# Performance work log

Measured on AMD Instinct MI355X. Metric: run time of the kernel, lower is better.

The kernel has to match this reference:

```python
import jax, jax.numpy as jnp
import numpy as np

N_HEAD = 16
N_EMBD = 768
HEAD_DIM = N_EMBD // N_HEAD  # 48


def setup_inputs() -> dict:
    key = jax.random.key(0)
    k1, k2, k3 = jax.random.split(key, 3)
    B, T, C = 4, 2048, N_EMBD
    x = jax.random.normal(k1, (B, T, C), dtype=jnp.float32)
    # nn.Linear(n_embd, 3*n_embd, bias=False): y = x @ W_attn, stored as [C, 3C]
    W_attn = jax.random.normal(k2, (C, 3 * C), dtype=jnp.float32) * (C ** -0.5)
    W_proj = jax.random.normal(k3, (C, C), dtype=jnp.float32) * (C ** -0.5)
    b_proj = jnp.zeros((C,), dtype=jnp.float32)
    return {"x": x, "W_attn": W_attn, "W_proj": W_proj, "b_proj": b_proj}


def reference(x, W_attn, W_proj, b_proj):
    B, T, C = x.shape
    qkv = x @ W_attn  # [B, T, 3C]
    q, k, v = jnp.split(qkv, 3, axis=-1)
    # [B, T, H, D]
    q = q.reshape(B, T, N_HEAD, HEAD_DIM)
    k = k.reshape(B, T, N_HEAD, HEAD_DIM)
    v = v.reshape(B, T, N_HEAD, HEAD_DIM)
    scale = HEAD_DIM ** -0.5
    # scores: [B, H, Tq, Tk]
    wei = jnp.einsum("bqhd,bkhd->bhqk", q, k) * scale
    causal = jnp.tril(jnp.ones((T, T), dtype=bool))
    wei = jnp.where(causal[None, None, :, :], wei, -jnp.inf)
    wei = jax.nn.softmax(wei, axis=-1)
    # dropout omitted (eval mode / deterministic reference)
    out = jnp.einsum("bhqk,bkhd->bqhd", wei, v).reshape(B, T, C)
    return out @ W_proj + b_proj
```

## Files before the change

### kernel.cpp

```cpp
#include <hip/hip_runtime.h>
#include <cstdint>
#include <cstddef>

#define B_ 4
#define T_ 2048
#define C_ 768
#define H_ 16
#define D_ 48
#define M_ (B_*T_)
#define N3_ (3*C_)

typedef unsigned short u16;
typedef __attribute__((ext_vector_type(8))) short bf16x8;
typedef __attribute__((ext_vector_type(4))) float f32x4;
typedef __attribute__((ext_vector_type(4))) unsigned int u32x4;
typedef __attribute__((ext_vector_type(4))) unsigned short u16x4;

typedef const __attribute__((address_space(1))) unsigned int* gptr_t;
typedef __attribute__((address_space(3))) unsigned int* lptr_t;

__device__ __forceinline__ u16 f2b(float f){
  union { float f; unsigned u; } x; x.f = f;
  unsigned u = x.u;
  return (u16)((u + 0x7FFFu + ((u >> 16) & 1u)) >> 16);
}

__device__ __forceinline__ unsigned cvtpk(float lo, float hi){
  unsigned r;
  asm("v_cvt_pk_bf16_f32 %0, %1, %2" : "=v"(r) : "v"(lo), "v"(hi));
  return r;
}

__device__ __forceinline__ bf16x8 ld_frag(const u16* lds, int row, int kbyte){
  const char* p = (const char*)lds + (row << 7) + (kbyte ^ ((row & 7) << 4));
  return *(const bf16x8*)p;
}

__device__ __forceinline__ bf16x8 ld_k(const u16* kb, int rbase, int off){
  return *(const bf16x8*)((const char*)kb + rbase + off);
}

__global__ void k_cvt(const float* __restrict__ in, u16* __restrict__ out, int n4){
  int i = blockIdx.x * blockDim.x + threadIdx.x;
  if (i >= n4) return;
  f32x4 v = *(const f32x4*)(in + 4*(size_t)i);
  u16x4 o;
  o.x = f2b(v.x); o.y = f2b(v.y); o.z = f2b(v.z); o.w = f2b(v.w);
  *(u16x4*)(out + 4*(size_t)i) = o;
}

__global__ void k_tpose(const float* __restrict__ in, u16* __restrict__ out, int R, int Cn,
                        int scaleRows, float scl){
  __shared__ float tile[32][33];
  int tx = threadIdx.x & 31, ty = threadIdx.x >> 5;
  int c  = blockIdx.x * 32 + tx;
  int rb = blockIdx.y * 32;
  #pragma unroll
  for (int r0 = 0; r0 < 32; r0 += 8)
    tile[ty + r0][tx] = in[(size_t)(rb + ty + r0) * Cn + c];
  __syncthreads();
  int oc = rb + tx;
  int cb = blockIdx.x * 32;
  #pragma unroll
  for (int r0 = 0; r0 < 32; r0 += 8){
    float v = tile[tx][ty + r0];
    if (cb + ty + r0 < scaleRows) v *= scl;
    out[(size_t)(cb + ty + r0) * R + oc] = f2b(v);
  }
}

template<bool OUT_BF16, bool ADD_BIAS>
__launch_bounds__(256)
__global__ void k_gemm(const u16* __restrict__ A, const u16* __restrict__ Bt,
                       void* __restrict__ Cout, const float* __restrict__ bias,
                       int Ndim, int Kdim){
  __shared__ u16 lA[128*64];
  __shared__ u16 lB[128*64];
  const int tid = threadIdx.x, lane = tid & 63, w = tid >> 6;
  const int m0 = blockIdx.x * 128, n0 = blockIdx.y * 128;
  const int wr = (w >> 1) * 64, wc = (w & 1) * 64;
  const f32x4 fzero = {0.f, 0.f, 0.f, 0.f};
  f32x4 acc[4][4];
  #pragma unroll
  for (int i = 0; i < 4; ++i)
    #pragma unroll
    for (int j = 0; j < 4; ++j) acc[i][j] = fzero;

  for (int k0 = 0; k0 < Kdim; k0 += 64){
    __syncthreads();
    #pragma unroll
    for (int it = 0; it < 4; ++it){
      int c = tid + it * 256;
      int row  = c >> 3;
      int cb   = (c & 7) << 4;
      int pcol = cb ^ ((row & 7) << 4);
      const char* ga = (const char*)(A  + (size_t)(m0 + row) * Kdim + k0) + pcol;
      const char* gb = (const char*)(Bt + (size_t)(n0 + row) * Kdim + k0) + pcol;
      __builtin_amdgcn_global_load_lds((gptr_t)ga, (lptr_t)((char*)lA + (c << 4)), 16, 0, 0);
      __builtin_amdgcn_global_load_lds((gptr_t)gb, (lptr_t)((char*)lB + (c << 4)), 16, 0, 0);
    }
    __syncthreads();
    #pragma unroll
    for (int kk = 0; kk < 2; ++kk){
      int kbyte = (kk << 6) + ((lane >> 4) << 4);
      bf16x8 af[4], bfv[4];
      #pragma unroll
      for (int i = 0; i < 4; ++i){
        af[i]  = ld_frag(lA, wr + i*16 + (lane & 15), kbyte);
        bfv[i] = ld_frag(lB, wc + i*16 + (lane & 15), kbyte);
      }
      #pragma unroll
      for (int i = 0; i < 4; ++i)
        #pragma unroll
        for (int j = 0; j < 4; ++j)
          acc[i][j] = __builtin_amdgcn_mfma_f32_16x16x32_bf16(af[i], bfv[j], acc[i][j], 0, 0, 0);
    }
  }
  #pragma unroll
  for (int i = 0; i < 4; ++i){
    int rbase = m0 + wr + i*16 + ((lane >> 4) << 2);
    #pragma unroll
    for (int j = 0; j < 4; ++j){
      int col = n0 + wc + j*16 + (lane & 15);
      float bv = ADD_BIAS ? bias[col] : 0.f;
      #pragma unroll
      for (int r = 0; r < 4; ++r){
        float v = acc[i][j][r] + bv;
        if (OUT_BF16) ((u16*)Cout)[(size_t)(rbase + r) * Ndim + col] = f2b(v);
        else          ((float*)Cout)[(size_t)(rbase + r) * Ndim + col] = v;
      }
    }
  }
}

__global__ void k_vt(const u16* __restrict__ qkv, u16* __restrict__ vt){
  __shared__ u16 tl[64][50];
  int t0 = blockIdx.x * 64;
  int bh = blockIdx.y; int b = bh >> 4, h = bh & 15;
  int tid = threadIdx.x;
  for (int i = tid; i < 64*48; i += 256){
    int tt = i / 48, d = i % 48;
    tl[tt][d] = qkv[(size_t)(b*T_ + t0 + tt) * N3_ + 2*C_ + h*D_ + d];
  }
  __syncthreads();
  for (int i = tid; i < 48*64; i += 256){
    int d = i >> 6, tt = i & 63;
    vt[(size_t)(bh*D_ + d) * T_ + t0 + tt] = tl[tt][d];
  }
}

__launch_bounds__(256)
__global__ void k_attn(const u16* __restrict__ qkv, const u16* __restrict__ vt,
                       u16* __restrict__ ao){
  __shared__ u16 lKV[2][2][6144];

  const int wg = ((blockIdx.x & 7) << 7) + (blockIdx.x >> 3);
  const int q  = wg & 127;
  const int pairI = q >> 3;
  const int bh = ((wg >> 7) << 3) + (q & 7);
  const int qbA = pairI, qbB = 31 - pairI;
  const int b = bh >> 4, h = bh & 15;
  const int tid = threadIdx.x, lane = tid & 63, w = tid >> 6;
  const int ls = lane & 15, hi = lane >> 4;
  const int krb = ls * 96 + hi * 16;
  const f32x4 fzero = {0.f, 0.f, 0.f, 0.f};
  const bf16x8 bzero = {0, 0, 0, 0, 0, 0, 0, 0};

  bf16x8 aqA[2], aqB[2];
  {
    const u16* qpA = qkv + (size_t)(b*T_ + qbA*64 + w*16 + ls) * N3_ + h*D_ + hi*8;
    aqA[0] = *(const bf16x8*)qpA;
    aqA[1] = (hi < 2) ? *(const bf16x8*)(qpA + 32) : bzero;
    const u16* qpB = qkv + (size_t)(b*T_ + qbB*64 + w*16 + ls) * N3_ + h*D_ + hi*8;
    aqB[0] = *(const bf16x8*)qpB;
    aqB[1] = (hi < 2) ? *(const bf16x8*)(qpB + 32) : bzero;
  }

  const char* kg0; const char* kg1; const char* vg;
  {
    int c0 = tid,       r0 = c0 / 6, i0 = (c0 % 6) << 4;
    int c1 = tid + 256, r1 = c1 / 6, i1 = (c1 % 6) << 4;
    kg0 = (const char*)(qkv + (size_t)(b*T_ + r0) * N3_ + C_ + h*D_) + i0;
    kg1 = (const char*)(qkv + (size_t)(b*T_ + r1) * N3_ + C_ + h*D_) + i1;
    int d0  = tid >> 5;
    int pb4 = (tid << 2) & 127;
    int lb  = pb4 ^ (d0 << 4);
    int k   = lb >> 1;
    int sk  = (k & 0x23) | ((k & 4) << 2) | ((k & 0x18) >> 1);
    vg = (const char*)(vt + (size_t)(bh*D_ + d0) * T_) + (sk << 1);
  }
  const size_t kstep = (size_t)64 * N3_ * 2;

  auto STAGE1 = [&](int s, int buf, int sl){
    const size_t ko = (size_t)s * kstep;
    const int vo = s * 128;
    char* base = (char*)&lKV[buf][sl][0];
    __builtin_amdgcn_global_load_lds((gptr_t)(kg0 + ko), (lptr_t)(base + (tid << 4)), 16, 0, 0);
    if (tid < 128)
      __builtin_amdgcn_global_load_lds((gptr_t)(kg1 + ko), (lptr_t)(base + ((tid + 256) << 4)), 16, 0, 0);
    char* vd = base + 6144;
    #pragma unroll
    for (int it = 0; it < 6; ++it)
      __builtin_amdgcn_global_load_lds((gptr_t)(vg + vo + it * (8 * T_ * 2)),
          (lptr_t)(vd + ((tid + it*256) << 2)), 4, 0, 0);
  };

  float lsumA = 0.f, lsumB = 0.f;
  f32x4 oaccA[3], oaccB[3];
  #pragma unroll
  for (int nf = 0; nf < 3; ++nf){ oaccA[nf] = fzero; oaccB[nf] = fzero; }

  int cur = 0;

  auto softmax = [&](f32x4 (&s)[4], float &lsum,
                     bf16x8 &pb0, bf16x8 &pb1, bool diag, int krow0, int qt){
    if (diag){
      int qg = qt + w*16 + ls;
      #pragma unroll
      for (int nf = 0; nf < 4; ++nf)
        #pragma unroll
        for (int r = 0; r < 4; ++r){
          int kg2 = krow0 + nf*16 + hi*4 + r;
          s[nf][r] = (kg2 <= qg) ? s[nf][r] : -1e30f;
        }
    }
    float p[4][4];
    #pragma unroll
    for (int nf = 0; nf < 4; ++nf)
      #pragma unroll
      for (int r = 0; r < 4; ++r){
        float e = __builtin_amdgcn_exp2f(fminf(s[nf][r], 60.f));
        p[nf][r] = e;
        lsum += e;
      }
    union { u32x4 u; bf16x8 b; } w0, w1;
    w0.u.x = cvtpk(p[0][0], p[0][1]); w0.u.y = cvtpk(p[0][2], p[0][3]);
    w0.u.z = cvtpk(p[1][0], p[1][1]); w0.u.w = cvtpk(p[1][2], p[1][3]);
    w1.u.x = cvtpk(p[2][0], p[2][1]); w1.u.y = cvtpk(p[2][2], p[2][3]);
    w1.u.z = cvtpk(p[3][0], p[3][1]); w1.u.w = cvtpk(p[3][2], p[3][3]);
    pb0 = w0.b; pb1 = w1.b;
  };

  auto process = [&](int ks, int sl){
    const bool actA = (ks <= qbA);
    const u16* Kb = &lKV[cur][sl][0];
    const u16* Vb = Kb + 3072;

    f32x4 stA[4], stB[4];
    #pragma unroll
    for (int nf = 0; nf < 4; ++nf){ stA[nf] = fzero; stB[nf] = fzero; }
    #pragma unroll
    for (int kk = 0; kk < 2; ++kk){
      #pragma unroll
      for (int nf = 0; nf < 4; ++nf){
        bf16x8 bk = ld_k(Kb, krb, nf*1536 + (kk << 6));
        stB[nf] = __builtin_amdgcn_mfma_f32_16x16x32_bf16(bk, aqB[kk], stB[nf], 0, 0, 0);
        if (actA)
          stA[nf] = __builtin_amdgcn_mfma_f32_16x16x32_bf16(bk, aqA[kk], stA[nf], 0, 0, 0);
      }
    }

    bf16x8 pbA0, pbA1, pbB0, pbB1;
    if (actA) softmax(stA, lsumA, pbA0, pbA1, ks == qbA, ks*64, qbA*64);
    softmax(stB, lsumB, pbB0, pbB1, ks == qbB, ks*64, qbB*64);

    #pragma unroll
    for (int kk = 0; kk < 2; ++kk){
      int kbyte = (kk << 6) + (hi << 4);
      #pragma unroll
      for (int nf = 0; nf < 3; ++nf){
        bf16x8 bv = ld_frag(Vb, nf*16 + ls, kbyte);
        oaccB[nf] = __builtin_amdgcn_mfma_f32_16x16x32_bf16(
            bv, kk ? pbB1 : pbB0, oaccB[nf], 0, 0, 0);
        if (actA)
          oaccA[nf] = __builtin_amdgcn_mfma_f32_16x16x32_bf16(
              bv, kk ? pbA1 : pbA0, oaccA[nf], 0, 0, 0);
      }
    }
  };

  const int kb2max = qbB >> 1;
  STAGE1(0, 0, 0);
  if (qbB >= 1) STAGE1(1, 0, 1);
  __syncthreads();

  for (int kb2 = 0; kb2 <= kb2max; ++kb2){
    if (kb2 < kb2max){
      STAGE1(2*kb2 + 2, cur ^ 1, 0);
      if (2*kb2 + 3 <= qbB) STAGE1(2*kb2 + 3, cur ^ 1, 1);
    }

    process(2*kb2, 0);
    if (2*kb2 + 1 <= qbB) process(2*kb2 + 1, 1);

    if (kb2 < kb2max){
      __syncthreads();
      cur ^= 1;
    }
  }

  float lA = lsumA; lA += __shfl_xor(lA, 16); lA += __shfl_xor(lA, 32);
  float lB = lsumB; lB += __shfl_xor(lB, 16); lB += __shfl_xor(lB, 32);
  float invA = 1.f / lA, invB = 1.f / lB;
  int tA = qbA*64 + w*16 + ls, tB = qbB*64 + w*16 + ls;
  #pragma unroll
  for (int nf = 0; nf < 3; ++nf){
    u16x4 oA, oB;
    #pragma unroll
    for (int r = 0; r < 4; ++r){
      oA[r] = f2b(oaccA[nf][r] * invA);
      oB[r] = f2b(oaccB[nf][r] * invB);
    }
    int col = h*D_ + nf*16 + hi*4;
    *(u16x4*)(ao + (size_t)(b*T_ + tA) * C_ + col) = oA;
    *(u16x4*)(ao + (size_t)(b*T_ + tB) * C_ + col) = oB;
  }
}

extern "C" void kernel_launch(void* const* d_in, const int* in_sizes, int n_in,
                              void* d_out, int out_size, void* d_ws, size_t ws_size,
                              hipStream_t stream){
  if (n_in < 4) return;
  const float* x      = (const float*)d_in[0];
  const float* W_attn = (const float*)d_in[1];
  const float* W_proj = (const float*)d_in[2];
  const float* b_proj = (const float*)d_in[3];

  char* ws = (char*)d_ws;
  size_t off = 0;
  auto alloc = [&](size_t bytes)->void*{
    void* p = ws + off; off += (bytes + 255) & ~(size_t)255; return p;
  };
  u16* xb   = (u16*)alloc((size_t)M_ * C_  * 2);
  u16* wabT = (u16*)alloc((size_t)N3_ * C_ * 2);
  u16* wpbT = (u16*)alloc((size_t)C_ * C_  * 2);
  u16* qkv  = (u16*)alloc((size_t)M_ * N3_ * 2);
  u16* vt   = (u16*)alloc((size_t)B_ * H_ * D_ * T_ * 2);
  u16* ao   = (u16*)alloc((size_t)M_ * C_  * 2);
  if (off > ws_size) return;

  const float scale2 = 0.20823527f;

  k_cvt<<<dim3((M_*C_/4 + 255)/256), dim3(256), 0, stream>>>(x, xb, M_*C_/4);
  k_tpose<<<dim3(N3_/32, C_/32), dim3(256), 0, stream>>>(W_attn, wabT, C_, N3_, C_, scale2);
  k_tpose<<<dim3(C_/32,  C_/32), dim3(256), 0, stream>>>(W_proj, wpbT, C_, C_, 0, 1.f);
  k_gemm<true,false><<<dim3(M_/128, N3_/128), dim3(256), 0, stream>>>(
      xb, wabT, (void*)qkv, (const float*)nullptr, N3_, C_);
  k_vt<<<dim3(T_/64, B_*H_), dim3(256), 0, stream>>>(qkv, vt);
  k_attn<<<dim3(1024), dim3(256), 0, stream>>>(qkv, vt, ao);
  k_gemm<false,true><<<dim3(M_/128, C_/128), dim3(256), 0, stream>>>(
      ao, wpbT, d_out, b_proj, C_, C_);
}
```

Measured before the change: 140.2 us.

## Merge preprocessing kernels into one launch and shrink GEMM tiles to 64x128

The x bf16 conversion and both weight transposes now run in a single launch, split by block index ranges, which removes two kernel launches and their gaps. Both GEMMs now use 64x128 tiles, with each wave computing a 64x32 slice, in place of 128x128 tiles. This doubles the block count for better CU occupancy, especially for the projection GEMM's small grid, at the cost of less data reuse per block and more redundant B-tile loads.

```diff
diff --git a/kernel.cpp b/kernel.cpp
--- a/kernel.cpp
+++ b/kernel.cpp
@@ -40,27 +40,19 @@
   return *(const bf16x8*)((const char*)kb + rbase + off);
 }
 
-__global__ void k_cvt(const float* __restrict__ in, u16* __restrict__ out, int n4){
-  int i = blockIdx.x * blockDim.x + threadIdx.x;
-  if (i >= n4) return;
-  f32x4 v = *(const f32x4*)(in + 4*(size_t)i);
-  u16x4 o;
-  o.x = f2b(v.x); o.y = f2b(v.y); o.z = f2b(v.z); o.w = f2b(v.w);
-  *(u16x4*)(out + 4*(size_t)i) = o;
-}
-
-__global__ void k_tpose(const float* __restrict__ in, u16* __restrict__ out, int R, int Cn,
-                        int scaleRows, float scl){
+__device__ __forceinline__ void tpose_body(const float* __restrict__ in,
+                                           u16* __restrict__ out, int R, int Cn,
+                                           int bx, int by, int scaleRows, float scl){
   __shared__ float tile[32][33];
   int tx = threadIdx.x & 31, ty = threadIdx.x >> 5;
-  int c  = blockIdx.x * 32 + tx;
-  int rb = blockIdx.y * 32;
+  int c  = bx * 32 + tx;
+  int rb = by * 32;
   #pragma unroll
   for (int r0 = 0; r0 < 32; r0 += 8)
     tile[ty + r0][tx] = in[(size_t)(rb + ty + r0) * Cn + c];
   __syncthreads();
   int oc = rb + tx;
-  int cb = blockIdx.x * 32;
+  int cb = bx * 32;
   #pragma unroll
   for (int r0 = 0; r0 < 32; r0 += 8){
     float v = tile[tx][ty + r0];
@@ -69,59 +61,82 @@
   }
 }
 
+__global__ void k_prep(const float* __restrict__ x, u16* __restrict__ xb,
+                       const float* __restrict__ Wa, u16* __restrict__ wabT,
+                       const float* __restrict__ Wp, u16* __restrict__ wpbT,
+                       float scl){
+  int blk = blockIdx.x;
+  if (blk < 6144){
+    int i = blk * 256 + threadIdx.x;
+    f32x4 v = *(const f32x4*)(x + 4*(size_t)i);
+    u16x4 o;
+    o.x = f2b(v.x); o.y = f2b(v.y); o.z = f2b(v.z); o.w = f2b(v.w);
+    *(u16x4*)(xb + 4*(size_t)i) = o;
+  } else if (blk < 7872){
+    int id = blk - 6144;
+    tpose_body(Wa, wabT, C_, N3_, id % 72, id / 72, C_, scl);
+  } else {
+    int id = blk - 7872;
+    tpose_body(Wp, wpbT, C_, C_, id % 24, id / 24, 0, 1.f);
+  }
+}
+
 template<bool OUT_BF16, bool ADD_BIAS>
 __launch_bounds__(256)
-__global__ void k_gemm(const u16* __restrict__ A, const u16* __restrict__ Bt,
-                       void* __restrict__ Cout, const float* __restrict__ bias,
-                       int Ndim, int Kdim){
-  __shared__ u16 lA[128*64];
+__global__ void k_gemm2(const u16* __restrict__ A, const u16* __restrict__ Bt,
+                        void* __restrict__ Cout, const float* __restrict__ bias,
+                        int Ndim, int Kdim){
+  __shared__ u16 lA[64*64];
   __shared__ u16 lB[128*64];
   const int tid = threadIdx.x, lane = tid & 63, w = tid >> 6;
-  const int m0 = blockIdx.x * 128, n0 = blockIdx.y * 128;
-  const int wr = (w >> 1) * 64, wc = (w & 1) * 64;
+  const int m0 = blockIdx.x * 64, n0 = blockIdx.y * 128;
+  const int wc = w * 32;
+  const int ls = lane & 15, hi = lane >> 4;
   const f32x4 fzero = {0.f, 0.f, 0.f, 0.f};
-  f32x4 acc[4][4];
-  #pragma unroll
-  for (int i = 0; i < 4; ++i)
-    #pragma unroll
-    for (int j = 0; j < 4; ++j) acc[i][j] = fzero;
+  f32x4 acc[4][2];
+  #pragma unroll
+  for (int i = 0; i < 4; ++i){ acc[i][0] = fzero; acc[i][1] = fzero; }
 
   for (int k0 = 0; k0 < Kdim; k0 += 64){
     __syncthreads();
     #pragma unroll
+    for (int it = 0; it < 2; ++it){
+      int c = tid + it * 256;
+      int row = c >> 3, cb = (c & 7) << 4;
+      int pcol = cb ^ ((row & 7) << 4);
+      const char* ga = (const char*)(A + (size_t)(m0 + row) * Kdim + k0) + pcol;
+      __builtin_amdgcn_global_load_lds((gptr_t)ga, (lptr_t)((char*)lA + (c << 4)), 16, 0, 0);
+    }
+    #pragma unroll
     for (int it = 0; it < 4; ++it){
       int c = tid + it * 256;
-      int row  = c >> 3;
-      int cb   = (c & 7) << 4;
+      int row = c >> 3, cb = (c & 7) << 4;
       int pcol = cb ^ ((row & 7) << 4);
-      const char* ga = (const char*)(A  + (size_t)(m0 + row) * Kdim + k0) + pcol;
       const char* gb = (const char*)(Bt + (size_t)(n0 + row) * Kdim + k0) + pcol;
-      __builtin_amdgcn_global_load_lds((gptr_t)ga, (lptr_t)((char*)lA + (c << 4)), 16, 0, 0);
       __builtin_amdgcn_global_load_lds((gptr_t)gb, (lptr_t)((char*)lB + (c << 4)), 16, 0, 0);
     }
     __syncthreads();
     #pragma unroll
     for (int kk = 0; kk < 2; ++kk){
-      int kbyte = (kk << 6) + ((lane >> 4) << 4);
-      bf16x8 af[4], bfv[4];
-      #pragma unroll
-      for (int i = 0; i < 4; ++i){
-        af[i]  = ld_frag(lA, wr + i*16 + (lane & 15), kbyte);
-        bfv[i] = ld_frag(lB, wc + i*16 + (lane & 15), kbyte);
-      }
+      int kbyte = (kk << 6) + (hi << 4);
+      bf16x8 af[4], bfv[2];
+      #pragma unroll
+      for (int i = 0; i < 4; ++i) af[i] = ld_frag(lA, i*16 + ls, kbyte);
+      #pragma unroll
+      for (int j = 0; j < 2; ++j) bfv[j] = ld_frag(lB, wc + j*16 + ls, kbyte);
       #pragma unroll
       for (int i = 0; i < 4; ++i)
         #pragma unroll
-        for (int j = 0; j < 4; ++j)
+        for (int j = 0; j < 2; ++j)
           acc[i][j] = __builtin_amdgcn_mfma_f32_16x16x32_bf16(af[i], bfv[j], acc[i][j], 0, 0, 0);
     }
   }
   #pragma unroll
   for (int i = 0; i < 4; ++i){
-    int rbase = m0 + wr + i*16 + ((lane >> 4) << 2);
-    #pragma unroll
-    for (int j = 0; j < 4; ++j){
-      int col = n0 + wc + j*16 + (lane & 15);
+    int rbase = m0 + i*16 + (hi << 2);
+    #pragma unroll
+    for (int j = 0; j < 2; ++j){
+      int col = n0 + wc + j*16 + ls;
       float bv = ADD_BIAS ? bias[col] : 0.f;
       #pragma unroll
       for (int r = 0; r < 4; ++r){
@@ -341,13 +356,11 @@
 
   const float scale2 = 0.20823527f;
 
-  k_cvt<<<dim3((M_*C_/4 + 255)/256), dim3(256), 0, stream>>>(x, xb, M_*C_/4);
-  k_tpose<<<dim3(N3_/32, C_/32), dim3(256), 0, stream>>>(W_attn, wabT, C_, N3_, C_, scale2);
-  k_tpose<<<dim3(C_/32,  C_/32), dim3(256), 0, stream>>>(W_proj, wpbT, C_, C_, 0, 1.f);
-  k_gemm<true,false><<<dim3(M_/128, N3_/128), dim3(256), 0, stream>>>(
+  k_prep<<<dim3(8448), dim3(256), 0, stream>>>(x, xb, W_attn, wabT, W_proj, wpbT, scale2);
+  k_gemm2<true,false><<<dim3(M_/64, N3_/128), dim3(256), 0, stream>>>(
       xb, wabT, (void*)qkv, (const float*)nullptr, N3_, C_);
   k_vt<<<dim3(T_/64, B_*H_), dim3(256), 0, stream>>>(qkv, vt);
   k_attn<<<dim3(1024), dim3(256), 0, stream>>>(qkv, vt, ao);
-  k_gemm<false,true><<<dim3(M_/128, C_/128), dim3(256), 0, stream>>>(
+  k_gemm2<false,true><<<dim3(M_/64, C_/128), dim3(256), 0, stream>>>(
       ao, wpbT, d_out, b_proj, C_, C_);
 }
```

New measurement: 136.0 us. 1.03x faster.
